# Kernel optimization log

Measured on AMD Instinct MI355X. Metric: run time of the kernel, lower is better.

The kernel has to match this reference:

```python
import jax, jax.numpy as jnp
import numpy as np

T = 120  # hard-coded timestep count in the original forward


def gru_scan(x, W_ih, W_hh, b_ih, b_hh):
    """Run a torch-style GRUCell over time. x: [B, T, D] -> outputs [B, T, H]."""
    B = x.shape[0]
    H = W_hh.shape[1]

    def step(h, xt):
        gi = xt @ W_ih.T + b_ih          # [B, 3H]
        gh = h @ W_hh.T + b_hh           # [B, 3H]
        i_r, i_z, i_n = jnp.split(gi, 3, axis=-1)
        h_r, h_z, h_n = jnp.split(gh, 3, axis=-1)
        r = jax.nn.sigmoid(i_r + h_r)
        z = jax.nn.sigmoid(i_z + h_z)
        n = jnp.tanh(i_n + r * h_n)
        h_new = (1.0 - z) * n + z * h
        return h_new, h_new

    h0 = jnp.zeros((B, H), x.dtype)
    _, ys = jax.lax.scan(step, h0, jnp.swapaxes(x, 0, 1))  # ys: [T, B, H]
    return jnp.swapaxes(ys, 0, 1)


def setup_inputs() -> dict:
    key = jax.random.key(0)
    ks = jax.random.split(key, 20)
    B, Dc, Da, H, A = 2048, 128, 96, 256, 40
    s = 0.05
    inp = {
        "crime_input": jax.random.normal(ks[0], (B, T, Dc), jnp.float32),
        "anomaly_input": jax.random.normal(ks[1], (B, T, Da), jnp.float32),
        # gru_crime
        "W_ih_c": jax.random.normal(ks[2], (3 * H, Dc), jnp.float32) * s,
        "W_hh_c": jax.random.normal(ks[3], (3 * H, H), jnp.float32) * s,
        "b_ih_c": jax.random.normal(ks[4], (3 * H,), jnp.float32) * s,
        "b_hh_c": jax.random.normal(ks[5], (3 * H,), jnp.float32) * s,
        # gru_anomaly
        "W_ih_a": jax.random.normal(ks[6], (3 * H, Da), jnp.float32) * s,
        "W_hh_a": jax.random.normal(ks[7], (3 * H, H), jnp.float32) * s,
        "b_ih_a": jax.random.normal(ks[8], (3 * H,), jnp.float32) * s,
        "b_hh_a": jax.random.normal(ks[9], (3 * H,), jnp.float32) * s,
        # gru_inter (input = 2H)
        "W_ih_i": jax.random.normal(ks[10], (3 * H, 2 * H), jnp.float32) * s,
        "W_hh_i": jax.random.normal(ks[11], (3 * H, H), jnp.float32) * s,
        "b_ih_i": jax.random.normal(ks[12], (3 * H,), jnp.float32) * s,
        "b_hh_i": jax.random.normal(ks[13], (3 * H,), jnp.float32) * s,
        # attention
        "Wv": jax.random.normal(ks[14], (A, H), jnp.float32) * s,
        "bv": jax.random.normal(ks[15], (A,), jnp.float32) * s,
        "wu": jax.random.normal(ks[16], (A,), jnp.float32) * s,
    }
    return inp


def reference(crime_input, anomaly_input,
              W_ih_c, W_hh_c, b_ih_c, b_hh_c,
              W_ih_a, W_hh_a, b_ih_a, b_hh_a,
              W_ih_i, W_hh_i, b_ih_i, b_hh_i,
              Wv, bv, wu):
    # dropout layers are identity in eval mode
    out_c = gru_scan(crime_input, W_ih_c, W_hh_c, b_ih_c, b_hh_c)      # [B,T,H]
    out_a = gru_scan(anomaly_input, W_ih_a, W_hh_a, b_ih_a, b_hh_a)    # [B,T,H]
    inp_i = jnp.concatenate([out_c, out_a], axis=2)                    # [B,T,2H]
    out_i = gru_scan(inp_i, W_ih_i, W_hh_i, b_ih_i, b_hh_i)            # [B,T,H]

    um = jnp.tanh(jnp.einsum('bth,ah->bta', out_i, Wv) + bv)           # [B,T,A]
    scores = jnp.einsum('bta,a->bt', um, wu)                           # [B,T]
    alpha = jax.nn.softmax(scores, axis=1)                             # [B,T]
    context = jnp.einsum('bt,bth->bh', alpha, out_i)[:, None, :]       # [B,1,H]
    return context
```

## Files before the change

kernel.cpp:

```cpp
#include <hip/hip_runtime.h>

typedef float  f32x4  __attribute__((ext_vector_type(4)));
typedef short  short8 __attribute__((ext_vector_type(8)));
typedef __bf16 bf16x8 __attribute__((ext_vector_type(8)));

#define B_SZ 2048
#define T_SZ 120
#define H_SZ 256
#define G3   768
#define A_SZ 40

#define MFMA_BF16 __builtin_amdgcn_mfma_f32_16x16x32_bf16

union U8 { short8 s; bf16x8 b; };
__device__ __forceinline__ bf16x8 as_bf(short8 s){ U8 u; u.s = s; return u.b; }

__device__ __forceinline__ unsigned short f2bf(float x){
  unsigned u = __float_as_uint(x);
  return (unsigned short)((u + 0x7FFFu + ((u >> 16) & 1u)) >> 16);
}
__device__ __forceinline__ float bf2f(unsigned short h){
  return __uint_as_float(((unsigned)h) << 16);
}
__device__ __forceinline__ void cvt_hilo(float x, short& hi, short& lo){
  unsigned short h = f2bf(x);
  hi = (short)h;
  lo = (short)f2bf(x - bf2f(h));
}
__device__ __forceinline__ float sigm(float x){ return 1.0f / (1.0f + __expf(-x)); }
__device__ __forceinline__ float tanh_(float x){
  float a = fabsf(x);
  float t = 1.0f - 2.0f / (__expf(2.0f * a) + 1.0f);
  return copysignf(t, x);
}

__global__ void zinit(float* __restrict__ p, size_t n){
  size_t i = (size_t)blockIdx.x * 256 + threadIdx.x;
  size_t stride = (size_t)gridDim.x * 256;
  for (; i < n; i += stride) p[i] = 0.0f;
}

__global__ void packall(const float* __restrict__ WihC, const float* __restrict__ WhhC,
                        const float* __restrict__ WihA, const float* __restrict__ WhhA,
                        const float* __restrict__ WihI, const float* __restrict__ WhhI,
                        const float* __restrict__ Wv,
                        short* __restrict__ pIhC, short* __restrict__ pHhC,
                        short* __restrict__ pIhA, short* __restrict__ pHhA,
                        short* __restrict__ pIhI, short* __restrict__ pHhI,
                        short* __restrict__ pWvT)
{
  int b = blockIdx.x;
  int lane = threadIdx.x;
  const float* src; short* dst; int K;
  if      (b < 192)  { src = WihC; dst = pIhC; K = 128; }
  else if (b < 576)  { b -= 192;  src = WhhC; dst = pHhC; K = 256; }
  else if (b < 720)  { b -= 576;  src = WihA; dst = pIhA; K = 96;  }
  else if (b < 1104) { b -= 720;  src = WhhA; dst = pHhA; K = 256; }
  else if (b < 1872) { b -= 1104; src = WihI; dst = pIhI; K = 512; }
  else if (b < 2256) { b -= 1872; src = WhhI; dst = pHhI; K = 256; }
  else {
    int bb = b - 2256;
    int q = bb >> 3, kt = bb & 7;
    int a = q * 16 + (lane & 15);
    int k = kt * 32 + (lane >> 4) * 8;
    size_t o = (((size_t)q * 8 + kt) * 64 + lane) * 8;
#pragma unroll
    for (int i = 0; i < 8; i++){
      float v = (a < A_SZ) ? Wv[(size_t)a * H_SZ + k + i] : 0.0f;
      pWvT[o + i] = (short)f2bf(v);
    }
    return;
  }
  int KT = K >> 5;
  int nt = b / KT, kt = b % KT;
  const float* s = src + (size_t)(nt * 16 + (lane & 15)) * K + kt * 32 + (lane >> 4) * 8;
  size_t o = (((size_t)nt * KT + kt) * 64 + lane) * 8;
#pragma unroll
  for (int i = 0; i < 8; i++) dst[o + i] = (short)f2bf(s[i]);
}

__device__ __forceinline__ void gemm_body(
    int bid, const short* __restrict__ A, const short* __restrict__ Bhi,
    const float* __restrict__ b1, const float* __restrict__ b2,
    float* __restrict__ C, short* Ash)
{
  int tid = threadIdx.x;
  int w = tid >> 6, lane = tid & 63;
  int mg = w & 1, ng = w >> 1;
  int m0 = bid * 64;
  int nb = ng * 12;
  const int KT = 16;

  {
    int r = tid >> 3, s0 = (tid & 7) * 64;
    const short* src = A + (size_t)(m0 + r) * 512 + s0;
    short* dst = Ash + r * 520 + s0;
#pragma unroll
    for (int i = 0; i < 8; i++)
      *(short8*)(dst + i * 8) = *(const short8*)(src + i * 8);
  }
  __syncthreads();

  const f32x4 zero = {0.f, 0.f, 0.f, 0.f};
  f32x4 acc[2][12];
#pragma unroll
  for (int f = 0; f < 2; f++)
#pragma unroll
    for (int q = 0; q < 12; q++) acc[f][q] = zero;

  int rr = lane & 15, ks = lane >> 4;
  const short* Ap[2];
#pragma unroll
  for (int f = 0; f < 2; f++)
    Ap[f] = Ash + (mg * 32 + f * 16 + rr) * 520 + ks * 8;

  for (int kt = 0; kt < KT; ++kt){
    bf16x8 ahb[2];
#pragma unroll
    for (int f = 0; f < 2; f++)
      ahb[f] = as_bf(*(const short8*)(Ap[f] + kt * 32));
#pragma unroll
    for (int q = 0; q < 12; q++){
      int bo = (((nb + q) * KT + kt) * 64 + lane) * 8;
      bf16x8 bh = as_bf(*(const short8*)(Bhi + bo));
#pragma unroll
      for (int f = 0; f < 2; f++)
        acc[f][q] = MFMA_BF16(ahb[f], bh, acc[f][q], 0, 0, 0);
    }
  }
  int nc = lane & 15;
  int rb = lane >> 4;
#pragma unroll
  for (int q = 0; q < 12; q++){
    int n = (nb + q) * 16 + nc;
    float bias = b1[n] + (n < 512 ? b2[n] : 0.0f);
#pragma unroll
    for (int f = 0; f < 2; f++)
#pragma unroll
      for (int i = 0; i < 4; i++)
        C[(size_t)(m0 + mg * 32 + f * 16 + rb * 4 + i) * G3 + n] = acc[f][q][i] + bias;
  }
}

template<int D, int KI>
__device__ __forceinline__ void leaf32_body(
    const float* __restrict__ x, const short* __restrict__ Wih,
    const short* __restrict__ Whh, const float* __restrict__ bih,
    const float* __restrict__ bhh, short* __restrict__ outp, int ooff,
    float* __restrict__ hs, int b0, int t0, int tcnt,
    short* hhi, short* hlo, short* xhi)
{
  constexpr int XP  = D + 8;
  constexpr int NST = 4 * D;
  constexpr int CPR = D / 8;
  int tid = threadIdx.x, w = tid >> 6, lane = tid & 63;
  int arow = lane & 15, kgrp = lane >> 4;
  int c0 = w * 16 + arow;
  int msk = (arow & 7) << 4;

  float bir[2], biz[2], bin_[2], bhn[2];
#pragma unroll
  for (int j = 0; j < 2; j++){
    int c = c0 + j * 128;
    bir[j] = bih[c] + bhh[c];
    biz[j] = bih[256 + c] + bhh[256 + c];
    bin_[j] = bih[512 + c];
    bhn[j] = bhh[512 + c];
  }

  int srow = tid / CPR, scol = (tid % CPR) * 8;
  bool stg = tid < NST;
  const float* sx = x + ((size_t)(b0 + srow) * T_SZ + t0) * D + scol;
  short* xwh = xhi + srow * XP + scol;

  int orow = tid >> 4, ocb = (tid & 15) * 16;
  const char* ord0 = (const char*)hhi + orow * 512 + ((ocb * 2) ^ ((orow & 7) << 4));
  const char* ord1 = (const char*)hhi + orow * 512 + (((ocb + 8) * 2) ^ ((orow & 7) << 4));
  short* owp = outp + (size_t)(b0 + orow) * tcnt * 512 + ooff + ocb;

  float hreg[2][2][4];
#pragma unroll
  for (int f = 0; f < 2; f++)
#pragma unroll
  for (int j = 0; j < 2; j++)
#pragma unroll
  for (int i = 0; i < 4; i++){
    int row = f * 16 + kgrp * 4 + i, c = c0 + j * 128;
    float v = hs[(size_t)(b0 + row) * H_SZ + c];
    hreg[f][j][i] = v;
    short h_, l_; cvt_hilo(v, h_, l_);
    int off = row * 512 + ((c * 2) ^ ((row & 7) << 4));
    *(short*)((char*)hhi + off) = h_;
    *(short*)((char*)hlo + off) = l_;
  }
  if (stg){
    f32x4 a0 = *(const f32x4*)sx;
    f32x4 a1 = *(const f32x4*)(sx + 4);
    short8 h8;
#pragma unroll
    for (int i = 0; i < 4; i++){ h8[i] = (short)f2bf(a0[i]); h8[4+i] = (short)f2bf(a1[i]); }
    *(short8*)xwh = h8;
  }
  __syncthreads();

  const char *hhp[2], *hlp[2], *xhp[2];
#pragma unroll
  for (int f = 0; f < 2; f++){
    hhp[f] = (const char*)hhi + (f * 16 + arow) * 512;
    hlp[f] = (const char*)hlo + (f * 16 + arow) * 512;
    xhp[f] = (const char*)xhi + ((f * 16 + arow) * XP + kgrp * 8) * 2;
  }

  const f32x4 zero = {0.f, 0.f, 0.f, 0.f};
  for (int t = 0; t < tcnt; t++){
    if (t > 0){
      *(short8*)(owp + (size_t)(t - 1) * 512) = *(const short8*)ord0;
      *(short8*)(owp + (size_t)(t - 1) * 512 + 8) = *(const short8*)ord1;
    }

    f32x4 acc[2][6], accNi[2][2];
#pragma unroll
    for (int f = 0; f < 2; f++){
#pragma unroll
      for (int q = 0; q < 6; q++) acc[f][q] = zero;
      accNi[f][0] = zero; accNi[f][1] = zero;
    }

#pragma unroll
    for (int kt = 0; kt < KI; kt++){
      short8 wb[6];
#pragma unroll
      for (int q = 0; q < 6; q++)
        wb[q] = *(const short8*)(Wih + (((w + 8 * q) * KI + kt) * 64 + lane) * 8);
      bf16x8 ah[2];
#pragma unroll
      for (int f = 0; f < 2; f++)
        ah[f] = as_bf(*(const short8*)(xhp[f] + kt * 64));
#pragma unroll
      for (int q = 0; q < 6; q++){
        bf16x8 bw = as_bf(wb[q]);
#pragma unroll
        for (int f = 0; f < 2; f++){
          if (q < 4) acc[f][q] = MFMA_BF16(ah[f], bw, acc[f][q], 0, 0, 0);
          else       accNi[f][q-4] = MFMA_BF16(ah[f], bw, accNi[f][q-4], 0, 0, 0);
        }
      }
    }
#pragma unroll
    for (int kt = 0; kt < 8; kt++){
      short8 wb[6];
#pragma unroll
      for (int q = 0; q < 6; q++)
        wb[q] = *(const short8*)(Whh + (((w + 8 * q) * 8 + kt) * 64 + lane) * 8);
      int kb = (kt * 64 + kgrp * 16) ^ msk;
      bf16x8 ah[2], al[2];
#pragma unroll
      for (int f = 0; f < 2; f++){
        ah[f] = as_bf(*(const short8*)(hhp[f] + kb));
        al[f] = as_bf(*(const short8*)(hlp[f] + kb));
      }
#pragma unroll
      for (int q = 0; q < 6; q++){
        bf16x8 bw = as_bf(wb[q]);
#pragma unroll
        for (int f = 0; f < 2; f++){
          acc[f][q] = MFMA_BF16(ah[f], bw, acc[f][q], 0, 0, 0);
          acc[f][q] = MFMA_BF16(al[f], bw, acc[f][q], 0, 0, 0);
        }
      }
    }
    __syncthreads();

    f32x4 a0, a1;
    bool ds = stg && (t + 1 < tcnt);
    if (ds){
      a0 = *(const f32x4*)(sx + (size_t)(t + 1) * D);
      a1 = *(const f32x4*)(sx + (size_t)(t + 1) * D + 4);
    }

#pragma unroll
    for (int f = 0; f < 2; f++)
#pragma unroll
    for (int j = 0; j < 2; j++)
#pragma unroll
    for (int i = 0; i < 4; i++){
      float rr = sigm(acc[f][j][i] + bir[j]);
      float zz = sigm(acc[f][2 + j][i] + biz[j]);
      float nn = tanh_(accNi[f][j][i] + bin_[j] + rr * (acc[f][4 + j][i] + bhn[j]));
      float hv = (1.0f - zz) * nn + zz * hreg[f][j][i];
      hreg[f][j][i] = hv;
      int row = f * 16 + kgrp * 4 + i, c = c0 + j * 128;
      short h_, l_; cvt_hilo(hv, h_, l_);
      int off = row * 512 + ((c * 2) ^ ((row & 7) << 4));
      *(short*)((char*)hhi + off) = h_;
      *(short*)((char*)hlo + off) = l_;
    }
    if (ds){
      short8 h8;
#pragma unroll
      for (int i = 0; i < 4; i++){ h8[i] = (short)f2bf(a0[i]); h8[4+i] = (short)f2bf(a1[i]); }
      *(short8*)xwh = h8;
    }
    __syncthreads();
  }

  *(short8*)(owp + (size_t)(tcnt - 1) * 512) = *(const short8*)ord0;
  *(short8*)(owp + (size_t)(tcnt - 1) * 512 + 8) = *(const short8*)ord1;

#pragma unroll
  for (int f = 0; f < 2; f++)
#pragma unroll
  for (int j = 0; j < 2; j++)
#pragma unroll
  for (int i = 0; i < 4; i++){
    int row = f * 16 + kgrp * 4 + i;
    hs[(size_t)(b0 + row) * H_SZ + c0 + j * 128] = hreg[f][j][i];
  }
}

__device__ __forceinline__ void inter_body(
    int bid, const float* __restrict__ gi,
    const short* __restrict__ Whh, const float* __restrict__ bhh,
    const short* __restrict__ WvT,
    const float* __restrict__ bv, const float* __restrict__ wu,
    float* __restrict__ ctx, float* __restrict__ lsum,
    float* __restrict__ hs, int tcnt,
    short* hhi, short* hlo, short* wvl, float* esh)
{
  int b0 = bid * 16;
  int tid = threadIdx.x, w = tid >> 6, lane = tid & 63;
  int arow = lane & 15, kgrp = lane >> 4;
  int c0 = w * 16 + arow;
  int msk = (arow & 7) << 4;

  float bhn[2];
  bhn[0] = bhh[512 + c0];
  bhn[1] = bhh[512 + c0 + 128];

  float wuv[3], bvv[3];
#pragma unroll
  for (int q = 0; q < 3; q++){
    int a = q * 16 + arow;
    wuv[q] = (a < A_SZ) ? wu[a] : 0.0f;
    bvv[q] = (a < A_SZ) ? bv[a] : 0.0f;
  }

  for (int i = tid; i < 3 * 8 * 64; i += 512)
    *(short8*)(wvl + i * 8) = *(const short8*)(WvT + (size_t)i * 8);

  float hreg[2][4];
#pragma unroll
  for (int j = 0; j < 2; j++)
#pragma unroll
  for (int i = 0; i < 4; i++){
    int row = kgrp * 4 + i, c = c0 + j * 128;
    float v = hs[(size_t)(b0 + row) * H_SZ + c];
    hreg[j][i] = v;
    short h_, l_; cvt_hilo(v, h_, l_);
    int off = row * 512 + ((c * 2) ^ ((row & 7) << 4));
    *(short*)((char*)hhi + off) = h_;
    *(short*)((char*)hlo + off) = l_;
  }
  __syncthreads();

  const char* hhp = (const char*)hhi + arow * 512;
  const char* hlp = (const char*)hlo + arow * 512;
  const float* gp[4];
#pragma unroll
  for (int i = 0; i < 4; i++)
    gp[i] = gi + (size_t)(b0 + kgrp * 4 + i) * tcnt * G3;

  float ctxa[2][4] = {{0.f,0.f,0.f,0.f},{0.f,0.f,0.f,0.f}};
  float lsr[4] = {0.f, 0.f, 0.f, 0.f};

  const f32x4 zero = {0.f, 0.f, 0.f, 0.f};
  for (int t = 0; t < tcnt; t++){
    float gvr[2][4], gvz[2][4], gvn[2][4];
#pragma unroll
    for (int j = 0; j < 2; j++)
#pragma unroll
    for (int i = 0; i < 4; i++){
      const float* g = gp[i] + (size_t)t * G3 + c0 + j * 128;
      gvr[j][i] = g[0];
      gvz[j][i] = g[256];
      gvn[j][i] = g[512];
    }

    f32x4 acc[6];
#pragma unroll
    for (int q = 0; q < 6; q++) acc[q] = zero;

    short8 wb[6], wn[6];
#pragma unroll
    for (int q = 0; q < 6; q++)
      wb[q] = *(const short8*)(Whh + (((w + 8 * q) * 8) * 64 + lane) * 8);
#pragma unroll
    for (int kt = 0; kt < 8; kt++){
      if (kt < 7){
#pragma unroll
        for (int q = 0; q < 6; q++)
          wn[q] = *(const short8*)(Whh + (((w + 8 * q) * 8 + kt + 1) * 64 + lane) * 8);
      }
      int kb = (kt * 64 + kgrp * 16) ^ msk;
      bf16x8 ah = as_bf(*(const short8*)(hhp + kb));
      bf16x8 al = as_bf(*(const short8*)(hlp + kb));
#pragma unroll
      for (int q = 0; q < 6; q++){
        bf16x8 bw = as_bf(wb[q]);
        acc[q] = MFMA_BF16(ah, bw, acc[q], 0, 0, 0);
        acc[q] = MFMA_BF16(al, bw, acc[q], 0, 0, 0);
      }
      if (kt < 7){
#pragma unroll
        for (int q = 0; q < 6; q++) wb[q] = wn[q];
      }
    }

    if (w == 0 && t > 0){
      f32x4 um[3];
#pragma unroll
      for (int q = 0; q < 3; q++) um[q] = zero;
#pragma unroll
      for (int kt = 0; kt < 8; kt++){
        int kb = (kt * 64 + kgrp * 16) ^ msk;
        bf16x8 ah = as_bf(*(const short8*)(hhp + kb));
#pragma unroll
        for (int q = 0; q < 3; q++){
          bf16x8 bw = as_bf(*(const short8*)(wvl + ((q * 8 + kt) * 64 + lane) * 8));
          um[q] = MFMA_BF16(ah, bw, um[q], 0, 0, 0);
        }
      }
      f32x4 sp;
#pragma unroll
      for (int i = 0; i < 4; i++){
        float v = 0.f;
#pragma unroll
        for (int q = 0; q < 3; q++)
          v += wuv[q] * tanh_(um[q][i] + bvv[q]);
        sp[i] = v;
      }
#pragma unroll
      for (int d = 1; d < 16; d <<= 1){
#pragma unroll
        for (int i = 0; i < 4; i++)
          sp[i] += __shfl_xor(sp[i], d);
      }
      if (arow == 0){
#pragma unroll
        for (int i = 0; i < 4; i++){
          float e = __expf(sp[i]);
          esh[kgrp * 4 + i] = e;
          lsr[i] += e;
        }
      }
    }
    __syncthreads();

    if (t > 0){
#pragma unroll
      for (int i = 0; i < 4; i++){
        float e = esh[kgrp * 4 + i];
#pragma unroll
        for (int j = 0; j < 2; j++)
          ctxa[j][i] += e * hreg[j][i];
      }
    }

#pragma unroll
    for (int j = 0; j < 2; j++)
#pragma unroll
    for (int i = 0; i < 4; i++){
      float rr = sigm(gvr[j][i] + acc[j][i]);
      float zz = sigm(gvz[j][i] + acc[2 + j][i]);
      float nn = tanh_(gvn[j][i] + rr * (acc[4 + j][i] + bhn[j]));
      float hv = (1.0f - zz) * nn + zz * hreg[j][i];
      hreg[j][i] = hv;
      int row = kgrp * 4 + i, c = c0 + j * 128;
      short h_, l_; cvt_hilo(hv, h_, l_);
      int off = row * 512 + ((c * 2) ^ ((row & 7) << 4));
      *(short*)((char*)hhi + off) = h_;
      *(short*)((char*)hlo + off) = l_;
    }
    __syncthreads();
  }

  if (w == 0){
    f32x4 um[3];
#pragma unroll
    for (int q = 0; q < 3; q++) um[q] = zero;
#pragma unroll
    for (int kt = 0; kt < 8; kt++){
      int kb = (kt * 64 + kgrp * 16) ^ msk;
      bf16x8 ah = as_bf(*(const short8*)(hhp + kb));
#pragma unroll
      for (int q = 0; q < 3; q++){
        bf16x8 bw = as_bf(*(const short8*)(wvl + ((q * 8 + kt) * 64 + lane) * 8));
        um[q] = MFMA_BF16(ah, bw, um[q], 0, 0, 0);
      }
    }
    f32x4 sp;
#pragma unroll
    for (int i = 0; i < 4; i++){
      float v = 0.f;
#pragma unroll
      for (int q = 0; q < 3; q++)
        v += wuv[q] * tanh_(um[q][i] + bvv[q]);
      sp[i] = v;
    }
#pragma unroll
    for (int d = 1; d < 16; d <<= 1){
#pragma unroll
      for (int i = 0; i < 4; i++)
        sp[i] += __shfl_xor(sp[i], d);
    }
    if (arow == 0){
#pragma unroll
      for (int i = 0; i < 4; i++){
        float e = __expf(sp[i]);
        esh[kgrp * 4 + i] = e;
        lsr[i] += e;
      }
    }
  }
  __syncthreads();
#pragma unroll
  for (int i = 0; i < 4; i++){
    float e = esh[kgrp * 4 + i];
#pragma unroll
    for (int j = 0; j < 2; j++)
      ctxa[j][i] += e * hreg[j][i];
  }

#pragma unroll
  for (int j = 0; j < 2; j++)
#pragma unroll
  for (int i = 0; i < 4; i++){
    int row = kgrp * 4 + i;
    hs[(size_t)(b0 + row) * H_SZ + c0 + j * 128] = hreg[j][i];
    ctx[(size_t)(b0 + row) * H_SZ + c0 + j * 128] += ctxa[j][i];
  }
  if (w == 0 && arow == 0){
#pragma unroll
    for (int i = 0; i < 4; i++)
      lsum[b0 + kgrp * 4 + i] += lsr[i];
  }
}

__global__ __launch_bounds__(512, 2) void fused3(
    int nIb, int nLb,
    const float* __restrict__ giI, const short* __restrict__ WhhI_,
    const float* __restrict__ bhhI_, const short* __restrict__ WvT,
    const float* __restrict__ bv, const float* __restrict__ wu,
    float* __restrict__ ctx, float* __restrict__ lsum,
    float* __restrict__ hsI, int tcntI,
    const float* __restrict__ x0, const short* __restrict__ WihL0,
    const short* __restrict__ WhhL0, const float* __restrict__ bihL0,
    const float* __restrict__ bhhL0,
    const float* __restrict__ x1, const short* __restrict__ WihL1,
    const short* __restrict__ WhhL1, const float* __restrict__ bihL1,
    const float* __restrict__ bhhL1,
    short* __restrict__ outL, float* __restrict__ hsC, float* __restrict__ hsA,
    int t0L, int tcntL,
    const short* __restrict__ Ag, const short* __restrict__ BhiG,
    const float* __restrict__ b1G, const float* __restrict__ b2G,
    float* __restrict__ Cg)
{
  __shared__ short smem[64 * 520];
  int bid = blockIdx.x;
  if (bid < nIb){
    inter_body(bid, giI, WhhI_, bhhI_, WvT, bv, wu, ctx, lsum, hsI, tcntI,
               smem, smem + 4096, smem + 8192, (float*)(smem + 20480));
  } else if (bid < nIb + nLb){
    int lb = bid - nIb;
    short* hhi = smem;
    short* hlo = smem + 8192;
    short* xhi = smem + 16384;
    if (lb < 64)
      leaf32_body<128, 4>(x0, WihL0, WhhL0, bihL0, bhhL0, outL, 0, hsC,
                          lb * 32, t0L, tcntL, hhi, hlo, xhi);
    else
      leaf32_body<96, 3>(x1, WihL1, WhhL1, bihL1, bhhL1, outL, 256, hsA,
                         (lb - 64) * 32, t0L, tcntL, hhi, hlo, xhi);
  } else {
    gemm_body(bid - nIb - nLb, Ag, BhiG, b1G, b2G, Cg, smem);
  }
}

__global__ __launch_bounds__(256, 1) void attn_fin(
    const float* __restrict__ ctx, const float* __restrict__ lsum,
    float* __restrict__ out)
{
  int b = blockIdx.x, tid = threadIdx.x;
  out[(size_t)b * H_SZ + tid] = ctx[(size_t)b * H_SZ + tid] / lsum[b];
}

extern "C" void kernel_launch(void* const* d_in, const int* in_sizes, int n_in,
                              void* d_out, int out_size, void* d_ws, size_t ws_size,
                              hipStream_t stream)
{
  (void)in_sizes; (void)n_in; (void)out_size;
  const float* crime = (const float*)d_in[0];
  const float* anom  = (const float*)d_in[1];
  const float* WihC = (const float*)d_in[2];
  const float* WhhC = (const float*)d_in[3];
  const float* bihC = (const float*)d_in[4];
  const float* bhhC = (const float*)d_in[5];
  const float* WihA = (const float*)d_in[6];
  const float* WhhA = (const float*)d_in[7];
  const float* bihA = (const float*)d_in[8];
  const float* bhhA = (const float*)d_in[9];
  const float* WihI = (const float*)d_in[10];
  const float* WhhI = (const float*)d_in[11];
  const float* bihI = (const float*)d_in[12];
  const float* bhhI = (const float*)d_in[13];
  const float* Wv = (const float*)d_in[14];
  const float* bv = (const float*)d_in[15];
  const float* wu = (const float*)d_in[16];
  float* out = (float*)d_out;

  char* ws = (char*)d_ws;
  size_t off = 0;
  auto take = [&](size_t n){ size_t r = off; off += (n + 255) & ~(size_t)255; return r; };

  short* pIhC = (short*)(ws + take((size_t)G3 * 128 * 2));
  short* pHhC = (short*)(ws + take((size_t)G3 * 256 * 2));
  short* pIhA = (short*)(ws + take((size_t)G3 * 96 * 2));
  short* pHhA = (short*)(ws + take((size_t)G3 * 256 * 2));
  short* pIhI = (short*)(ws + take((size_t)G3 * 512 * 2));
  short* pHhI = (short*)(ws + take((size_t)G3 * 256 * 2));
  short* pWvT = (short*)(ws + take((size_t)3 * 8 * 64 * 8 * 2));

  size_t state_off = off;
  float* hsC  = (float*)(ws + take((size_t)B_SZ * H_SZ * 4));
  float* hsA  = (float*)(ws + take((size_t)B_SZ * H_SZ * 4));
  float* hsI  = (float*)(ws + take((size_t)B_SZ * H_SZ * 4));
  float* ctx  = (float*)(ws + take((size_t)B_SZ * H_SZ * 4));
  float* lsum = (float*)(ws + take((size_t)B_SZ * 4));
  size_t state_end = off;

  size_t per2 = (size_t)B_SZ * (G3 * 4 + 512 * 2) * 2;
  size_t avail = (ws_size > off + 8192) ? (ws_size - off - 8192) : 0;
  int TC = (int)(avail / per2);
  if (TC > 20) TC = 20;
  if (TC < 1) TC = 1;
  if (TC > T_SZ) TC = T_SZ;
  int nc = (T_SZ + TC - 1) / TC;

  float* Gi[2];  short* OcaH[2];
  Gi[0]   = (float*)(ws + take((size_t)B_SZ * TC * G3 * 4));
  Gi[1]   = (float*)(ws + take((size_t)B_SZ * TC * G3 * 4));
  OcaH[0] = (short*)(ws + take((size_t)B_SZ * TC * 512 * 2));
  OcaH[1] = (short*)(ws + take((size_t)B_SZ * TC * 512 * 2));

  auto tcn = [&](int j){
    if (j < 0 || j >= nc) return 0;
    int r = T_SZ - j * TC;
    return r < TC ? r : TC;
  };

  zinit<<<2048, 256, 0, stream>>>((float*)(ws + state_off), (state_end - state_off) / 4);
  packall<<<2280, 64, 0, stream>>>(WihC, WhhC, WihA, WhhA, WihI, WhhI, Wv,
                                   pIhC, pHhC, pIhA, pHhA, pIhI, pHhI, pWvT);

  for (int k = 0; k <= nc + 1; k++){
    int tL = tcn(k), tG = tcn(k - 1), tI = tcn(k - 2);
    int nLb = tL ? 128 : 0;
    int nGb = tG ? (B_SZ * tG) / 64 : 0;
    int nIb = tI ? 128 : 0;
    int grid = nIb + nLb + nGb;
    if (grid == 0) continue;
    fused3<<<grid, 512, 0, stream>>>(
        nIb, nLb,
        Gi[k & 1], pHhI, bhhI, pWvT, bv, wu, ctx, lsum, hsI, tI,
        crime, pIhC, pHhC, bihC, bhhC,
        anom,  pIhA, pHhA, bihA, bhhA,
        OcaH[k & 1], hsC, hsA, k * TC, tL,
        OcaH[(k - 1) & 1], pIhI, bihI, bhhI, Gi[(k - 1) & 1]);
  }
  attn_fin<<<B_SZ, 256, 0, stream>>>(ctx, lsum, out);
}
```

Baseline: 3.195 ms.

## Process 32 batch rows per inter-GRU block to reuse recurrent weights

The inter-layer GRU block now handles 32 batch rows instead of 16, so each recurrent weight fragment loaded from global memory feeds MFMAs for two row tiles, halving weight traffic per row. The attention score computation is split across two waves, one per 16-row half. Inter blocks drop from 128 to 64 per launch, which lowers parallelism on the critical recurrent path and raises register pressure. The next-step weight prefetch double-buffering is also removed.

New measurement: 3.558 ms. 11.4% more time.

```diff
diff --git a/kernel.cpp b/kernel.cpp
--- a/kernel.cpp
+++ b/kernel.cpp
@@ -318,7 +318,7 @@
   }
 }
 
-__device__ __forceinline__ void inter_body(
+__device__ __forceinline__ void inter32_body(
     int bid, const float* __restrict__ gi,
     const short* __restrict__ Whh, const float* __restrict__ bhh,
     const short* __restrict__ WvT,
@@ -327,11 +327,12 @@
     float* __restrict__ hs, int tcnt,
     short* hhi, short* hlo, short* wvl, float* esh)
 {
-  int b0 = bid * 16;
+  int b0 = bid * 32;
   int tid = threadIdx.x, w = tid >> 6, lane = tid & 63;
   int arow = lane & 15, kgrp = lane >> 4;
   int c0 = w * 16 + arow;
   int msk = (arow & 7) << 4;
+  bool att = (w < 2);
 
   float bhn[2];
   bhn[0] = bhh[512 + c0];
@@ -348,14 +349,16 @@
   for (int i = tid; i < 3 * 8 * 64; i += 512)
     *(short8*)(wvl + i * 8) = *(const short8*)(WvT + (size_t)i * 8);
 
-  float hreg[2][4];
+  float hreg[2][2][4];
+#pragma unroll
+  for (int f = 0; f < 2; f++)
 #pragma unroll
   for (int j = 0; j < 2; j++)
 #pragma unroll
   for (int i = 0; i < 4; i++){
-    int row = kgrp * 4 + i, c = c0 + j * 128;
+    int row = f * 16 + kgrp * 4 + i, c = c0 + j * 128;
     float v = hs[(size_t)(b0 + row) * H_SZ + c];
-    hreg[j][i] = v;
+    hreg[f][j][i] = v;
     short h_, l_; cvt_hilo(v, h_, l_);
     int off = row * 512 + ((c * 2) ^ ((row & 7) << 4));
     *(short*)((char*)hhi + off) = h_;
@@ -363,67 +366,77 @@
   }
   __syncthreads();
 
-  const char* hhp = (const char*)hhi + arow * 512;
-  const char* hlp = (const char*)hlo + arow * 512;
-  const float* gp[4];
+  const char *hhp[2], *hlp[2];
+#pragma unroll
+  for (int f = 0; f < 2; f++){
+    hhp[f] = (const char*)hhi + (f * 16 + arow) * 512;
+    hlp[f] = (const char*)hlo + (f * 16 + arow) * 512;
+  }
+  const char* ahp = (const char*)hhi + (((w & 1) * 16 + arow)) * 512;
+
+  const float* gp[2][4];
+#pragma unroll
+  for (int f = 0; f < 2; f++)
 #pragma unroll
   for (int i = 0; i < 4; i++)
-    gp[i] = gi + (size_t)(b0 + kgrp * 4 + i) * tcnt * G3;
-
-  float ctxa[2][4] = {{0.f,0.f,0.f,0.f},{0.f,0.f,0.f,0.f}};
+    gp[f][i] = gi + (size_t)(b0 + f * 16 + kgrp * 4 + i) * tcnt * G3;
+
+  float ctxa[2][2][4] = {};
   float lsr[4] = {0.f, 0.f, 0.f, 0.f};
 
   const f32x4 zero = {0.f, 0.f, 0.f, 0.f};
   for (int t = 0; t < tcnt; t++){
-    float gvr[2][4], gvz[2][4], gvn[2][4];
+    float gvr[2][2][4], gvz[2][2][4], gvn[2][2][4];
+#pragma unroll
+    for (int f = 0; f < 2; f++)
 #pragma unroll
     for (int j = 0; j < 2; j++)
 #pragma unroll
     for (int i = 0; i < 4; i++){
-      const float* g = gp[i] + (size_t)t * G3 + c0 + j * 128;
-      gvr[j][i] = g[0];
-      gvz[j][i] = g[256];
-      gvn[j][i] = g[512];
-    }
-
-    f32x4 acc[6];
-#pragma unroll
-    for (int q = 0; q < 6; q++) acc[q] = zero;
-
-    short8 wb[6], wn[6];
-#pragma unroll
-    for (int q = 0; q < 6; q++)
-      wb[q] = *(const short8*)(Whh + (((w + 8 * q) * 8) * 64 + lane) * 8);
+      const float* g = gp[f][i] + (size_t)t * G3 + c0 + j * 128;
+      gvr[f][j][i] = g[0];
+      gvz[f][j][i] = g[256];
+      gvn[f][j][i] = g[512];
+    }
+
+    f32x4 acc[2][6];
+#pragma unroll
+    for (int f = 0; f < 2; f++)
+#pragma unroll
+      for (int q = 0; q < 6; q++) acc[f][q] = zero;
+
 #pragma unroll
     for (int kt = 0; kt < 8; kt++){
-      if (kt < 7){
-#pragma unroll
-        for (int q = 0; q < 6; q++)
-          wn[q] = *(const short8*)(Whh + (((w + 8 * q) * 8 + kt + 1) * 64 + lane) * 8);
-      }
+      short8 wb[6];
+#pragma unroll
+      for (int q = 0; q < 6; q++)
+        wb[q] = *(const short8*)(Whh + (((w + 8 * q) * 8 + kt) * 64 + lane) * 8);
       int kb = (kt * 64 + kgrp * 16) ^ msk;
-      bf16x8 ah = as_bf(*(const short8*)(hhp + kb));
-      bf16x8 al = as_bf(*(const short8*)(hlp + kb));
+      bf16x8 ah[2], al[2];
+#pragma unroll
+      for (int f = 0; f < 2; f++){
+        ah[f] = as_bf(*(const short8*)(hhp[f] + kb));
+        al[f] = as_bf(*(const short8*)(hlp[f] + kb));
+      }
 #pragma unroll
       for (int q = 0; q < 6; q++){
         bf16x8 bw = as_bf(wb[q]);
-        acc[q] = MFMA_BF16(ah, bw, acc[q], 0, 0, 0);
-        acc[q] = MFMA_BF16(al, bw, acc[q], 0, 0, 0);
-      }
-      if (kt < 7){
-#pragma unroll
-        for (int q = 0; q < 6; q++) wb[q] = wn[q];
-      }
-    }
-
-    if (w == 0 && t > 0){
+#pragma unroll
+        for (int f = 0; f < 2; f++){
+          acc[f][q] = MFMA_BF16(ah[f], bw, acc[f][q], 0, 0, 0);
+          acc[f][q] = MFMA_BF16(al[f], bw, acc[f][q], 0, 0, 0);
+        }
+      }
+    }
+
+    if (att && t > 0){
       f32x4 um[3];
 #pragma unroll
       for (int q = 0; q < 3; q++) um[q] = zero;
 #pragma unroll
       for (int kt = 0; kt < 8; kt++){
         int kb = (kt * 64 + kgrp * 16) ^ msk;
-        bf16x8 ah = as_bf(*(const short8*)(hhp + kb));
+        bf16x8 ah = as_bf(*(const short8*)(ahp + kb));
 #pragma unroll
         for (int q = 0; q < 3; q++){
           bf16x8 bw = as_bf(*(const short8*)(wvl + ((q * 8 + kt) * 64 + lane) * 8));
@@ -449,7 +462,7 @@
 #pragma unroll
         for (int i = 0; i < 4; i++){
           float e = __expf(sp[i]);
-          esh[kgrp * 4 + i] = e;
+          esh[w * 16 + kgrp * 4 + i] = e;
           lsr[i] += e;
         }
       }
@@ -458,24 +471,28 @@
 
     if (t > 0){
 #pragma unroll
+      for (int f = 0; f < 2; f++)
+#pragma unroll
       for (int i = 0; i < 4; i++){
-        float e = esh[kgrp * 4 + i];
+        float e = esh[f * 16 + kgrp * 4 + i];
 #pragma unroll
         for (int j = 0; j < 2; j++)
-          ctxa[j][i] += e * hreg[j][i];
-      }
-    }
-
+          ctxa[f][j][i] += e * hreg[f][j][i];
+      }
+    }
+
+#pragma unroll
+    for (int f = 0; f < 2; f++)
 #pragma unroll
     for (int j = 0; j < 2; j++)
 #pragma unroll
     for (int i = 0; i < 4; i++){
-      float rr = sigm(gvr[j][i] + acc[j][i]);
-      float zz = sigm(gvz[j][i] + acc[2 + j][i]);
-      float nn = tanh_(gvn[j][i] + rr * (acc[4 + j][i] + bhn[j]));
-      float hv = (1.0f - zz) * nn + zz * hreg[j][i];
-      hreg[j][i] = hv;
-      int row = kgrp * 4 + i, c = c0 + j * 128;
+      float rr = sigm(gvr[f][j][i] + acc[f][j][i]);
+      float zz = sigm(gvz[f][j][i] + acc[f][2 + j][i]);
+      float nn = tanh_(gvn[f][j][i] + rr * (acc[f][4 + j][i] + bhn[j]));
+      float hv = (1.0f - zz) * nn + zz * hreg[f][j][i];
+      hreg[f][j][i] = hv;
+      int row = f * 16 + kgrp * 4 + i, c = c0 + j * 128;
       short h_, l_; cvt_hilo(hv, h_, l_);
       int off = row * 512 + ((c * 2) ^ ((row & 7) << 4));
       *(short*)((char*)hhi + off) = h_;
@@ -484,14 +501,14 @@
     __syncthreads();
   }
 
-  if (w == 0){
+  if (att){
     f32x4 um[3];
 #pragma unroll
     for (int q = 0; q < 3; q++) um[q] = zero;
 #pragma unroll
     for (int kt = 0; kt < 8; kt++){
       int kb = (kt * 64 + kgrp * 16) ^ msk;
-      bf16x8 ah = as_bf(*(const short8*)(hhp + kb));
+      bf16x8 ah = as_bf(*(const short8*)(ahp + kb));
 #pragma unroll
       for (int q = 0; q < 3; q++){
         bf16x8 bw = as_bf(*(const short8*)(wvl + ((q * 8 + kt) * 64 + lane) * 8));
@@ -517,32 +534,36 @@
 #pragma unroll
       for (int i = 0; i < 4; i++){
         float e = __expf(sp[i]);
-        esh[kgrp * 4 + i] = e;
+        esh[w * 16 + kgrp * 4 + i] = e;
         lsr[i] += e;
       }
     }
   }
   __syncthreads();
 #pragma unroll
+  for (int f = 0; f < 2; f++)
+#pragma unroll
   for (int i = 0; i < 4; i++){
-    float e = esh[kgrp * 4 + i];
+    float e = esh[f * 16 + kgrp * 4 + i];
 #pragma unroll
     for (int j = 0; j < 2; j++)
-      ctxa[j][i] += e * hreg[j][i];
-  }
-
+      ctxa[f][j][i] += e * hreg[f][j][i];
+  }
+
+#pragma unroll
+  for (int f = 0; f < 2; f++)
 #pragma unroll
   for (int j = 0; j < 2; j++)
 #pragma unroll
   for (int i = 0; i < 4; i++){
-    int row = kgrp * 4 + i;
-    hs[(size_t)(b0 + row) * H_SZ + c0 + j * 128] = hreg[j][i];
-    ctx[(size_t)(b0 + row) * H_SZ + c0 + j * 128] += ctxa[j][i];
-  }
-  if (w == 0 && arow == 0){
+    int row = f * 16 + kgrp * 4 + i;
+    hs[(size_t)(b0 + row) * H_SZ + c0 + j * 128] = hreg[f][j][i];
+    ctx[(size_t)(b0 + row) * H_SZ + c0 + j * 128] += ctxa[f][j][i];
+  }
+  if (att && arow == 0){
 #pragma unroll
     for (int i = 0; i < 4; i++)
-      lsum[b0 + kgrp * 4 + i] += lsr[i];
+      lsum[b0 + w * 16 + kgrp * 4 + i] += lsr[i];
   }
 }
 
@@ -568,8 +589,8 @@
   __shared__ short smem[64 * 520];
   int bid = blockIdx.x;
   if (bid < nIb){
-    inter_body(bid, giI, WhhI_, bhhI_, WvT, bv, wu, ctx, lsum, hsI, tcntI,
-               smem, smem + 4096, smem + 8192, (float*)(smem + 20480));
+    inter32_body(bid, giI, WhhI_, bhhI_, WvT, bv, wu, ctx, lsum, hsI, tcntI,
+                 smem, smem + 8192, smem + 16384, (float*)(smem + 28672));
   } else if (bid < nIb + nLb){
     int lb = bid - nIb;
     short* hhi = smem;
@@ -666,7 +687,7 @@
     int tL = tcn(k), tG = tcn(k - 1), tI = tcn(k - 2);
     int nLb = tL ? 128 : 0;
     int nGb = tG ? (B_SZ * tG) / 64 : 0;
-    int nIb = tI ? 128 : 0;
+    int nIb = tI ? 64 : 0;
     int grid = nIb + nLb + nGb;
     if (grid == 0) continue;
     fused3<<<grid, 512, 0, stream>>>(
```
